# Kernel optimization log

Hardware: AMD Instinct MI355X
Metric: run time of the kernel (lower is better)

## Reference

```python
import jax, jax.numpy as jnp
import numpy as np

N, E, G, H = 4096, 8192, 64, 128  # nodes, edges, graphs, hidden dim
NODE_DIM, EDGE_DIM = 11, 5


def _linear_params(key, fan_in, fan_out):
    kw, kb = jax.random.split(key)
    s = 1.0 / np.sqrt(fan_in)
    w = jax.random.uniform(kw, (fan_in, fan_out), minval=-s, maxval=s, dtype=jnp.float32)
    b = jax.random.uniform(kb, (fan_out,), minval=-s, maxval=s, dtype=jnp.float32)
    return w, b


def setup_inputs() -> dict:
    key = jax.random.key(0)
    ks = jax.random.split(key, 10)
    x = jax.random.normal(ks[0], (N, NODE_DIM), dtype=jnp.float32)
    edge_attr = jax.random.normal(ks[1], (E, EDGE_DIM), dtype=jnp.float32)
    edge_index = jax.random.randint(ks[2], (2, E), 0, N, dtype=jnp.int64)
    batch = jnp.sort(jax.random.randint(ks[3], (N,), 0, G, dtype=jnp.int64))
    # preprocess MLP: node_dim -> 128 -> 128
    p1_w, p1_b = _linear_params(ks[4], NODE_DIM, H)
    p2_w, p2_b = _linear_params(ks[5], H, H)
    # edge net: edge_dim -> 128 -> 256 -> 128 -> 128*128 (ReLU between, none after last)
    e1_w, e1_b = _linear_params(ks[6], EDGE_DIM, 128)
    e2_w, e2_b = _linear_params(ks[7], 128, 256)
    e3_w, e3_b = _linear_params(ks[8], 256, 128)
    e4_w, e4_b = _linear_params(ks[9], 128, H * H)
    return {"x": x, "edge_attr": edge_attr, "edge_index": edge_index, "batch": batch,
            "p1_w": p1_w, "p1_b": p1_b, "p2_w": p2_w, "p2_b": p2_b,
            "e1_w": e1_w, "e1_b": e1_b, "e2_w": e2_w, "e2_b": e2_b,
            "e3_w": e3_w, "e3_b": e3_b, "e4_w": e4_w, "e4_b": e4_b}


def reference(x, edge_attr, edge_index, batch,
              p1_w, p1_b, p2_w, p2_b,
              e1_w, e1_b, e2_w, e2_b, e3_w, e3_b, e4_w, e4_b):
    # node preprocess MLP (maps 11-dim features to 128 so NNConv dims are consistent)
    h = jax.nn.relu(x @ p1_w + p1_b) @ p2_w + p2_b  # [N, H]
    # edge network -> per-edge weight matrix [E, H, H]
    e = jax.nn.relu(edge_attr @ e1_w + e1_b)
    e = jax.nn.relu(e @ e2_w + e2_b)
    e = jax.nn.relu(e @ e3_w + e3_b)
    W = (e @ e4_w + e4_b).reshape(E, H, H)
    # NNConv (root_weight=False, bias=False, aggr='mean'):
    src, dst = edge_index[0], edge_index[1]
    msg = jnp.einsum('ei,eio->eo', h[src], W)  # gather + per-edge matmul, [E, H]
    agg = jax.ops.segment_sum(msg, dst, num_segments=N)
    cnt = jax.ops.segment_sum(jnp.ones((E,), msg.dtype), dst, num_segments=N)
    h_out = agg / jnp.maximum(cnt, 1.0)[:, None]  # scatter-mean, [N, H]
    # global add pool over graphs
    pooled = jax.ops.segment_sum(h_out, batch, num_segments=G)  # [G, H]
    return pooled
```

## Files before the change

### kernel.cpp

```cpp
#include <hip/hip_runtime.h>
#include <hip/hip_bf16.h>

#define N_NODES 4096
#define N_EDGES 8192
#define N_GRAPHS 64
#define HDIM 128

typedef __attribute__((ext_vector_type(8))) short bf16x8;
typedef __attribute__((ext_vector_type(4))) float f32x4;

static __device__ __forceinline__ unsigned short f2bf(float f) {
    unsigned u = __builtin_bit_cast(unsigned, f);
    u += 0x7fffu + ((u >> 16) & 1u);
    return (unsigned short)(u >> 16);
}
static __device__ __forceinline__ float bf2f(unsigned short s) {
    unsigned u = ((unsigned)s) << 16;
    return __builtin_bit_cast(float, u);
}

__global__ __launch_bounds__(256) void pre_kernel(
    const float* __restrict__ x, const float* __restrict__ p1w, const float* __restrict__ p1b,
    const float* __restrict__ p2w, const float* __restrict__ p2b, const float* __restrict__ e4b,
    unsigned short* __restrict__ h_bf, float* __restrict__ hb,
    const float* __restrict__ w4, unsigned short* __restrict__ w4perm,
    const float* __restrict__ w2, unsigned short* __restrict__ w2p,
    const float* __restrict__ w3, unsigned short* __restrict__ w3p)
{
    __shared__ __align__(16) char smem[33024];
    const int t = threadIdx.x;
    const int bid = blockIdx.x;

    if (bid < 256) {
        float (*xs)[11]  = (float(*)[11])smem;
        float (*l1t)[16] = (float(*)[16])(smem + 704);
        float (*hs)[16]  = (float(*)[16])(smem + 8896);
        const int nb = bid;

        for (int r = t; r < 16 * 11; r += 256) {
            int e = r / 11, d = r % 11;
            xs[e][d] = x[(nb * 16 + e) * 11 + d];
        }
        __syncthreads();
        {
            int j = t & 127;
            float wd[11];
            #pragma unroll
            for (int d = 0; d < 11; ++d) wd[d] = p1w[d * 128 + j];
            float bj = p1b[j];
            for (int p = 0; p < 8; ++p) {
                int e = p * 2 + (t >> 7);
                float acc = bj;
                #pragma unroll
                for (int d = 0; d < 11; ++d) acc += xs[e][d] * wd[d];
                l1t[j][e] = fmaxf(acc, 0.f);
            }
        }
        __syncthreads();
        {
            int j = t & 127, eh = t >> 7;
            float acc[8];
            float bj = p2b[j];
            #pragma unroll
            for (int r = 0; r < 8; ++r) acc[r] = bj;
            #pragma unroll 8
            for (int k = 0; k < 128; ++k) {
                float w = p2w[k * 128 + j];
                const float4* row = (const float4*)&l1t[k][eh * 8];
                float4 v0 = row[0], v1 = row[1];
                acc[0] += v0.x * w; acc[1] += v0.y * w; acc[2] += v0.z * w; acc[3] += v0.w * w;
                acc[4] += v1.x * w; acc[5] += v1.y * w; acc[6] += v1.z * w; acc[7] += v1.w * w;
            }
            #pragma unroll
            for (int r = 0; r < 8; ++r) {
                int e = eh * 8 + r;
                h_bf[(nb * 16 + e) * 128 + j] = f2bf(acc[r]);
                hs[j][e] = acc[r];
            }
        }
        __syncthreads();
        {
            int j = t & 127, eh = t >> 7;
            float acc[8] = {0.f,0.f,0.f,0.f,0.f,0.f,0.f,0.f};
            #pragma unroll 8
            for (int i = 0; i < 128; ++i) {
                float w = e4b[i * 128 + j];
                const float4* row = (const float4*)&hs[i][eh * 8];
                float4 v0 = row[0], v1 = row[1];
                acc[0] += v0.x * w; acc[1] += v0.y * w; acc[2] += v0.z * w; acc[3] += v0.w * w;
                acc[4] += v1.x * w; acc[5] += v1.y * w; acc[6] += v1.z * w; acc[7] += v1.w * w;
            }
            #pragma unroll
            for (int r = 0; r < 8; ++r) hb[(nb * 16 + eh * 8 + r) * 128 + j] = acc[r];
        }
    } else if (bid < 384) {
        unsigned short (*tt)[129] = (unsigned short(*)[129])smem;
        const int i = bid - 256;
        for (int r = t; r < 16384; r += 256) {
            int k = r >> 7, o = r & 127;
            tt[o][k] = f2bf(w4[k * 16384 + i * 128 + o]);
        }
        __syncthreads();
        for (int r = t; r < 16384; r += 256) {
            int o = r >> 7, k = r & 127;
            w4perm[((size_t)(o >> 5) * 128 + i) * 4352 + (size_t)(o & 31) * 136 + k] = tt[o][k];
        }
    } else if (bid < 386) {
        unsigned short (*tt)[129] = (unsigned short(*)[129])smem;
        const int oh = bid - 384;
        for (int r = t; r < 16384; r += 256) {
            int k = r >> 7, ol = r & 127;
            tt[ol][k] = f2bf(w2[k * 256 + oh * 128 + ol]);
        }
        __syncthreads();
        for (int r = t; r < 16384; r += 256) {
            int ol = r >> 7, k = r & 127;
            w2p[(oh * 128 + ol) * 136 + k] = tt[ol][k];
        }
    } else {
        unsigned short (*tt)[257] = (unsigned short(*)[257])smem;
        const int oh = bid - 386;
        for (int r = t; r < 16384; r += 256) {
            int k = r >> 6, ol = r & 63;
            tt[ol][k] = f2bf(w3[k * 128 + oh * 64 + ol]);
        }
        __syncthreads();
        for (int r = t; r < 16384; r += 256) {
            int ol = r >> 8, k = r & 255;
            w3p[(oh * 64 + ol) * 264 + k] = tt[ol][k];
        }
    }
}

__global__ __launch_bounds__(256, 2) void edge23_kernel(
    const float* __restrict__ ea, const float* __restrict__ w1, const float* __restrict__ b1,
    const float* __restrict__ b2, const float* __restrict__ b3,
    const unsigned short* __restrict__ w2p, const unsigned short* __restrict__ w3p,
    unsigned short* __restrict__ e3bf, float* __restrict__ aggz)
{
    const int t = threadIdx.x, bid = blockIdx.x;

    if (bid >= 512) {
        float4* dst = (float4*)aggz;
        const float4 z = make_float4(0.f, 0.f, 0.f, 0.f);
        for (int i = (bid - 512) * 256 + t; i < 132096; i += 128 * 256) dst[i] = z;
        return;
    }

    __shared__ __align__(16) float es[16][5];
    __shared__ __align__(16) unsigned short l1a[16 * 136];
    __shared__ __align__(16) unsigned short l2a[16 * 264];
    const int w = t >> 6, lane = t & 63, q = lane >> 4, l15 = lane & 15;
    const int e0 = bid * 16;
    const f32x4 zero4 = (f32x4){0.f, 0.f, 0.f, 0.f};

    for (int r = t; r < 80; r += 256) es[r / 5][r % 5] = ea[e0 * 5 + r];
    __syncthreads();
    {
        int j = t & 127, eh = t >> 7;
        float wd[5];
        #pragma unroll
        for (int d = 0; d < 5; ++d) wd[d] = w1[d * 128 + j];
        float bj = b1[j];
        #pragma unroll
        for (int p = 0; p < 8; ++p) {
            int e = eh * 8 + p;
            float acc = bj;
            #pragma unroll
            for (int d = 0; d < 5; ++d) acc += es[e][d] * wd[d];
            l1a[e * 136 + j] = f2bf(fmaxf(acc, 0.f));
        }
    }
    __syncthreads();

    bf16x8 afrag[4];
    #pragma unroll
    for (int s = 0; s < 4; ++s)
        afrag[s] = *(const bf16x8*)&l1a[l15 * 136 + s * 32 + q * 8];

    f32x4 acc[4];
    #pragma unroll
    for (int ob = 0; ob < 4; ++ob) acc[ob] = zero4;
    #pragma unroll
    for (int ob = 0; ob < 4; ++ob) {
        const int o = w * 64 + ob * 16 + l15;
        bf16x8 bfrag[4];
        #pragma unroll
        for (int s = 0; s < 4; ++s)
            bfrag[s] = *(const bf16x8*)(w2p + (size_t)o * 136 + s * 32 + q * 8);
        f32x4 tmp = __builtin_amdgcn_mfma_f32_16x16x32_bf16(afrag[0], bfrag[0], zero4, 0, 0, 0);
        tmp = __builtin_amdgcn_mfma_f32_16x16x32_bf16(afrag[1], bfrag[1], tmp, 0, 0, 0);
        tmp = __builtin_amdgcn_mfma_f32_16x16x32_bf16(afrag[2], bfrag[2], tmp, 0, 0, 0);
        acc[ob] = __builtin_amdgcn_mfma_f32_16x16x32_bf16(afrag[3], bfrag[3], tmp, 0, 0, 0);
    }
    #pragma unroll
    for (int ob = 0; ob < 4; ++ob) {
        int o = w * 64 + ob * 16 + l15;
        float bo = b2[o];
        #pragma unroll
        for (int r = 0; r < 4; ++r) {
            int e_loc = q * 4 + r;
            l2a[e_loc * 264 + o] = f2bf(fmaxf(acc[ob][r] + bo, 0.f));
        }
    }
    __syncthreads();

    f32x4 acc3[2];
    acc3[0] = zero4; acc3[1] = zero4;
    #pragma unroll
    for (int ks = 0; ks < 8; ++ks) {
        bf16x8 a3 = *(const bf16x8*)&l2a[l15 * 264 + ks * 32 + q * 8];
        #pragma unroll
        for (int ob = 0; ob < 2; ++ob) {
            const int o = w * 32 + ob * 16 + l15;
            bf16x8 bf = *(const bf16x8*)(w3p + (size_t)o * 264 + ks * 32 + q * 8);
            acc3[ob] = __builtin_amdgcn_mfma_f32_16x16x32_bf16(a3, bf, acc3[ob], 0, 0, 0);
        }
    }
    #pragma unroll
    for (int ob = 0; ob < 2; ++ob) {
        int o = w * 32 + ob * 16 + l15;
        float bo = b3[o];
        #pragma unroll
        for (int r = 0; r < 4; ++r) {
            int e = e0 + q * 4 + r;
            e3bf[(size_t)e * 128 + o] = f2bf(fmaxf(acc3[ob][r] + bo, 0.f));
        }
    }
}

__global__ __launch_bounds__(256, 3) void nnconv_kernel(
    const unsigned short* __restrict__ e3bf, const unsigned short* __restrict__ h_bf,
    const unsigned short* __restrict__ w4perm, const float* __restrict__ hb,
    const int* __restrict__ ei, float* __restrict__ agg, float* __restrict__ cnt)
{
    __shared__ __align__(16) float ht_f[64 * 64];
    __shared__ __align__(16) float red[2 * 64 * 16];
    const int t = threadIdx.x;
    const int bid = blockIdx.x;
    const int osplit = bid & 3;
    const int ksplit = (bid >> 2) & 1;
    const int etile  = bid >> 3;
    const int w = t >> 6, lane = t & 63, q = lane >> 4, l15 = lane & 15;
    const int og   = w & 1;
    const int kpar = w >> 1;
    const int e0 = etile * 64;
    const int o0 = osplit * 32;
    const int i0 = ksplit * 64;

    bf16x8 afrag[4][4];
    #pragma unroll
    for (int mb = 0; mb < 4; ++mb)
        #pragma unroll
        for (int s = 0; s < 4; ++s) {
            int row = e0 + mb * 16 + l15;
            afrag[mb][s] = *(const bf16x8*)(e3bf + (size_t)row * 128 + s * 32 + q * 8);
        }
    #pragma unroll
    for (int mb = 0; mb < 4; ++mb)
        #pragma unroll
        for (int s = 0; s < 4; ++s)
            asm volatile("" : "+v"(afrag[mb][s]));
    asm volatile("" ::: "memory");

    {
        int r = t >> 2, part = t & 3;
        int s = ei[e0 + r];
        #pragma unroll
        for (int u = 0; u < 2; ++u) {
            uint4 v = *(const uint4*)(h_bf + (size_t)s * 128 + i0 + part * 16 + u * 8);
            const unsigned short* pv = (const unsigned short*)&v;
            #pragma unroll
            for (int j = 0; j < 8; ++j)
                ht_f[(part * 16 + u * 8 + j) * 64 + r] = bf2f(pv[j]);
        }
    }

    f32x4 acc[4];
    #pragma unroll
    for (int mb = 0; mb < 4; ++mb) acc[mb] = (f32x4){0.f, 0.f, 0.f, 0.f};
    const f32x4 zero4 = (f32x4){0.f, 0.f, 0.f, 0.f};

    __syncthreads();

    const unsigned short* bbase =
        w4perm + ((size_t)osplit * 128 + i0 + kpar * 32) * 4352
               + (size_t)(og * 16 + l15) * 136 + q * 8;
    #pragma unroll 2
    for (int c = 0; c < 32; ++c) {
        const unsigned short* bp = bbase + (size_t)c * 4352;
        bf16x8 bfrag[4];
        #pragma unroll
        for (int s = 0; s < 4; ++s)
            bfrag[s] = *(const bf16x8*)(bp + s * 32);
        const int cg = kpar * 32 + c;
        #pragma unroll
        for (int mb = 0; mb < 4; ++mb) {
            f32x4 hv = *(const f32x4*)&ht_f[cg * 64 + mb * 16 + q * 4];
            f32x4 tmp = __builtin_amdgcn_mfma_f32_16x16x32_bf16(afrag[mb][0], bfrag[0], zero4, 0, 0, 0);
            tmp = __builtin_amdgcn_mfma_f32_16x16x32_bf16(afrag[mb][1], bfrag[1], tmp, 0, 0, 0);
            tmp = __builtin_amdgcn_mfma_f32_16x16x32_bf16(afrag[mb][2], bfrag[2], tmp, 0, 0, 0);
            tmp = __builtin_amdgcn_mfma_f32_16x16x32_bf16(afrag[mb][3], bfrag[3], tmp, 0, 0, 0);
            #pragma unroll
            for (int r = 0; r < 4; ++r)
                acc[mb][r] += hv[r] * tmp[r];
        }
    }

    if (kpar == 1) {
        #pragma unroll
        for (int mb = 0; mb < 4; ++mb)
            #pragma unroll
            for (int r = 0; r < 4; ++r)
                red[(og * 64 + mb * 16 + q * 4 + r) * 16 + l15] = acc[mb][r];
    }
    __syncthreads();
    if (kpar == 0) {
        #pragma unroll
        for (int mb = 0; mb < 4; ++mb) {
            #pragma unroll
            for (int r = 0; r < 4; ++r) {
                int e_loc = mb * 16 + q * 4 + r;
                int e = e0 + e_loc;
                int de = ei[N_EDGES + e];
                int se = ei[e];
                int o = o0 + og * 16 + l15;
                float v = acc[mb][r] + red[(og * 64 + e_loc) * 16 + l15];
                if (ksplit == 0) v += hb[(size_t)se * 128 + o];
                if (osplit == 0 && ksplit == 0 && og == 0 && l15 == 0)
                    atomicAdd(&cnt[de], 1.0f);
                atomicAdd(&agg[(size_t)de * 128 + o], v);
            }
        }
    }
}

__global__ __launch_bounds__(128) void pool_kernel(
    const float* __restrict__ agg, const float* __restrict__ cnt,
    const int* __restrict__ batch, float* __restrict__ out)
{
    const int g = blockIdx.x, t = threadIdx.x;
    int lo = 0, hi = N_NODES;
    while (lo < hi) { int m = (lo + hi) >> 1; if (batch[m] < g) lo = m + 1; else hi = m; }
    const int n_lo = lo;
    int lo2 = n_lo, hi2 = N_NODES;
    while (lo2 < hi2) { int m = (lo2 + hi2) >> 1; if (batch[m] < g + 1) lo2 = m + 1; else hi2 = m; }
    const int n_hi = lo2;

    float s0 = 0.f, s1 = 0.f, s2 = 0.f, s3 = 0.f;
    int n = n_lo;
    for (; n + 4 <= n_hi; n += 4) {
        float c0 = cnt[n], c1 = cnt[n + 1], c2 = cnt[n + 2], c3 = cnt[n + 3];
        float v0 = agg[(n    ) * 128 + t];
        float v1 = agg[(n + 1) * 128 + t];
        float v2 = agg[(n + 2) * 128 + t];
        float v3 = agg[(n + 3) * 128 + t];
        s0 += v0 / (c0 > 1.f ? c0 : 1.f);
        s1 += v1 / (c1 > 1.f ? c1 : 1.f);
        s2 += v2 / (c2 > 1.f ? c2 : 1.f);
        s3 += v3 / (c3 > 1.f ? c3 : 1.f);
    }
    for (; n < n_hi; ++n) {
        float c = cnt[n];
        s0 += agg[n * 128 + t] / (c > 1.f ? c : 1.f);
    }
    out[g * 128 + t] = (s0 + s1) + (s2 + s3);
}

extern "C" void kernel_launch(void* const* d_in, const int* in_sizes, int n_in,
                              void* d_out, int out_size, void* d_ws, size_t ws_size,
                              hipStream_t stream)
{
    const float* x     = (const float*)d_in[0];
    const float* ea    = (const float*)d_in[1];
    const int*   ei    = (const int*)d_in[2];
    const int*   batch = (const int*)d_in[3];
    const float* p1w   = (const float*)d_in[4];
    const float* p1b   = (const float*)d_in[5];
    const float* p2w   = (const float*)d_in[6];
    const float* p2b   = (const float*)d_in[7];
    const float* w1    = (const float*)d_in[8];
    const float* b1    = (const float*)d_in[9];
    const float* w2    = (const float*)d_in[10];
    const float* b2    = (const float*)d_in[11];
    const float* w3    = (const float*)d_in[12];
    const float* b3    = (const float*)d_in[13];
    const float* w4    = (const float*)d_in[14];
    const float* b4    = (const float*)d_in[15];
    float* out = (float*)d_out;
    (void)in_sizes; (void)n_in; (void)out_size; (void)ws_size;

    char* ws = (char*)d_ws;
    unsigned short* h_bf = (unsigned short*)(ws);
    unsigned short* e3bf = (unsigned short*)(ws + 1048576);
    float* hb            = (float*)(ws + 3145728);
    unsigned short* w4p  = (unsigned short*)(ws + 5242880);
    float* agg           = (float*)(ws + 9699328);
    float* cnt           = (float*)(ws + 11796480);
    unsigned short* w2p  = (unsigned short*)(ws + 11812864);
    unsigned short* w3p  = (unsigned short*)(ws + 11882496);

    pre_kernel<<<388, 256, 0, stream>>>(
        x, p1w, p1b, p2w, p2b, b4, h_bf, hb,
        w4, w4p, w2, w2p, w3, w3p);
    edge23_kernel<<<640, 256, 0, stream>>>(ea, w1, b1, b2, b3, w2p, w3p, e3bf, agg);
    nnconv_kernel<<<1024, 256, 0, stream>>>(e3bf, h_bf, w4p, hb, ei, agg, cnt);
    pool_kernel<<<N_GRAPHS, 128, 0, stream>>>(agg, cnt, batch, out);
}
```

Measured before the change: 176.3 us.

## Fuse edge MLP into preprocessing kernel and widen pool kernel

Merges the edge-network layers 1-3 into the preprocessing kernel as extra blocks. This removes one kernel launch and the separate W2/W3 transpose-to-bf16 pass: the edge blocks now read fp32 W2/W3 straight from global memory with strided scalar loads and convert them on the fly. The agg zeroing also moves into the fused kernel. The pool kernel goes from 128 to 512 threads per graph, with node rows split across 4 thread groups and reduced through shared memory. The trade-off is that each of the 512 edge blocks now repeats uncoalesced strided weight loads and conversions instead of loading pre-packed bf16 vectors.

```diff
diff --git a/kernel.cpp b/kernel.cpp
--- a/kernel.cpp
+++ b/kernel.cpp
@@ -19,23 +19,115 @@
     return __builtin_bit_cast(float, u);
 }
 
-__global__ __launch_bounds__(256) void pre_kernel(
+__global__ __launch_bounds__(256) void fused_pre_edge_kernel(
     const float* __restrict__ x, const float* __restrict__ p1w, const float* __restrict__ p1b,
     const float* __restrict__ p2w, const float* __restrict__ p2b, const float* __restrict__ e4b,
     unsigned short* __restrict__ h_bf, float* __restrict__ hb,
+    const float* __restrict__ ea, const float* __restrict__ w1, const float* __restrict__ b1,
+    const float* __restrict__ w2, const float* __restrict__ b2,
+    const float* __restrict__ w3, const float* __restrict__ b3,
+    unsigned short* __restrict__ e3bf,
     const float* __restrict__ w4, unsigned short* __restrict__ w4perm,
-    const float* __restrict__ w2, unsigned short* __restrict__ w2p,
-    const float* __restrict__ w3, unsigned short* __restrict__ w3p)
+    float* __restrict__ aggz)
 {
     __shared__ __align__(16) char smem[33024];
     const int t = threadIdx.x;
     const int bid = blockIdx.x;
 
-    if (bid < 256) {
+    if (bid < 512) {
+        float (*es)[5] = (float(*)[5])smem;
+        unsigned short* l1a = (unsigned short*)(smem + 320);
+        unsigned short* l2a = (unsigned short*)(smem + 4672);
+        const int w = t >> 6, lane = t & 63, q = lane >> 4, l15 = lane & 15;
+        const int e0 = bid * 16;
+        const f32x4 zero4 = (f32x4){0.f, 0.f, 0.f, 0.f};
+
+        for (int r = t; r < 80; r += 256) es[r / 5][r % 5] = ea[e0 * 5 + r];
+        __syncthreads();
+        {
+            int j = t & 127, eh = t >> 7;
+            float wd[5];
+            #pragma unroll
+            for (int d = 0; d < 5; ++d) wd[d] = w1[d * 128 + j];
+            float bj = b1[j];
+            #pragma unroll
+            for (int p = 0; p < 8; ++p) {
+                int e = eh * 8 + p;
+                float acc = bj;
+                #pragma unroll
+                for (int d = 0; d < 5; ++d) acc += es[e][d] * wd[d];
+                l1a[e * 136 + j] = f2bf(fmaxf(acc, 0.f));
+            }
+        }
+        __syncthreads();
+
+        bf16x8 afrag[4];
+        #pragma unroll
+        for (int s = 0; s < 4; ++s)
+            afrag[s] = *(const bf16x8*)&l1a[l15 * 136 + s * 32 + q * 8];
+
+        f32x4 acc[4];
+        #pragma unroll
+        for (int ob = 0; ob < 4; ++ob) acc[ob] = zero4;
+        #pragma unroll
+        for (int ob = 0; ob < 4; ++ob) {
+            const int o = w * 64 + ob * 16 + l15;
+            bf16x8 bfrag[4];
+            #pragma unroll
+            for (int s = 0; s < 4; ++s) {
+                const int kb = s * 32 + q * 8;
+                #pragma unroll
+                for (int kk = 0; kk < 8; ++kk)
+                    bfrag[s][kk] = (short)f2bf(w2[(kb + kk) * 256 + o]);
+            }
+            f32x4 tmp = __builtin_amdgcn_mfma_f32_16x16x32_bf16(afrag[0], bfrag[0], zero4, 0, 0, 0);
+            tmp = __builtin_amdgcn_mfma_f32_16x16x32_bf16(afrag[1], bfrag[1], tmp, 0, 0, 0);
+            tmp = __builtin_amdgcn_mfma_f32_16x16x32_bf16(afrag[2], bfrag[2], tmp, 0, 0, 0);
+            acc[ob] = __builtin_amdgcn_mfma_f32_16x16x32_bf16(afrag[3], bfrag[3], tmp, 0, 0, 0);
+        }
+        #pragma unroll
+        for (int ob = 0; ob < 4; ++ob) {
+            int o = w * 64 + ob * 16 + l15;
+            float bo = b2[o];
+            #pragma unroll
+            for (int r = 0; r < 4; ++r) {
+                int e_loc = q * 4 + r;
+                l2a[e_loc * 264 + o] = f2bf(fmaxf(acc[ob][r] + bo, 0.f));
+            }
+        }
+        __syncthreads();
+
+        f32x4 acc3[2];
+        acc3[0] = zero4; acc3[1] = zero4;
+        #pragma unroll
+        for (int ks = 0; ks < 8; ++ks) {
+            bf16x8 a3 = *(const bf16x8*)&l2a[l15 * 264 + ks * 32 + q * 8];
+            #pragma unroll
+            for (int ob = 0; ob < 2; ++ob) {
+                const int o = w * 32 + ob * 16 + l15;
+                bf16x8 bf;
+                const int kb = ks * 32 + q * 8;
+                #pragma unroll
+                for (int kk = 0; kk < 8; ++kk)
+                    bf[kk] = (short)f2bf(w3[(kb + kk) * 128 + o]);
+                acc3[ob] = __builtin_amdgcn_mfma_f32_16x16x32_bf16(a3, bf, acc3[ob], 0, 0, 0);
+            }
+        }
+        #pragma unroll
+        for (int ob = 0; ob < 2; ++ob) {
+            int o = w * 32 + ob * 16 + l15;
+            float bo = b3[o];
+            #pragma unroll
+            for (int r = 0; r < 4; ++r) {
+                int e = e0 + q * 4 + r;
+                e3bf[(size_t)e * 128 + o] = f2bf(fmaxf(acc3[ob][r] + bo, 0.f));
+            }
+        }
+    } else if (bid < 768) {
         float (*xs)[11]  = (float(*)[11])smem;
         float (*l1t)[16] = (float(*)[16])(smem + 704);
         float (*hs)[16]  = (float(*)[16])(smem + 8896);
-        const int nb = bid;
+        const int nb = bid - 512;
 
         for (int r = t; r < 16 * 11; r += 256) {
             int e = r / 11, d = r % 11;
@@ -93,9 +185,9 @@
             #pragma unroll
             for (int r = 0; r < 8; ++r) hb[(nb * 16 + eh * 8 + r) * 128 + j] = acc[r];
         }
-    } else if (bid < 384) {
+    } else if (bid < 896) {
         unsigned short (*tt)[129] = (unsigned short(*)[129])smem;
-        const int i = bid - 256;
+        const int i = bid - 768;
         for (int r = t; r < 16384; r += 256) {
             int k = r >> 7, o = r & 127;
             tt[o][k] = f2bf(w4[k * 16384 + i * 128 + o]);
@@ -105,127 +197,10 @@
             int o = r >> 7, k = r & 127;
             w4perm[((size_t)(o >> 5) * 128 + i) * 4352 + (size_t)(o & 31) * 136 + k] = tt[o][k];
         }
-    } else if (bid < 386) {
-        unsigned short (*tt)[129] = (unsigned short(*)[129])smem;
-        const int oh = bid - 384;
-        for (int r = t; r < 16384; r += 256) {
-            int k = r >> 7, ol = r & 127;
-            tt[ol][k] = f2bf(w2[k * 256 + oh * 128 + ol]);
-        }
-        __syncthreads();
-        for (int r = t; r < 16384; r += 256) {
-            int ol = r >> 7, k = r & 127;
-            w2p[(oh * 128 + ol) * 136 + k] = tt[ol][k];
-        }
     } else {
-        unsigned short (*tt)[257] = (unsigned short(*)[257])smem;
-        const int oh = bid - 386;
-        for (int r = t; r < 16384; r += 256) {
-            int k = r >> 6, ol = r & 63;
-            tt[ol][k] = f2bf(w3[k * 128 + oh * 64 + ol]);
-        }
-        __syncthreads();
-        for (int r = t; r < 16384; r += 256) {
-            int ol = r >> 8, k = r & 255;
-            w3p[(oh * 64 + ol) * 264 + k] = tt[ol][k];
-        }
-    }
-}
-
-__global__ __launch_bounds__(256, 2) void edge23_kernel(
-    const float* __restrict__ ea, const float* __restrict__ w1, const float* __restrict__ b1,
-    const float* __restrict__ b2, const float* __restrict__ b3,
-    const unsigned short* __restrict__ w2p, const unsigned short* __restrict__ w3p,
-    unsigned short* __restrict__ e3bf, float* __restrict__ aggz)
-{
-    const int t = threadIdx.x, bid = blockIdx.x;
-
-    if (bid >= 512) {
         float4* dst = (float4*)aggz;
         const float4 z = make_float4(0.f, 0.f, 0.f, 0.f);
-        for (int i = (bid - 512) * 256 + t; i < 132096; i += 128 * 256) dst[i] = z;
-        return;
-    }
-
-    __shared__ __align__(16) float es[16][5];
-    __shared__ __align__(16) unsigned short l1a[16 * 136];
-    __shared__ __align__(16) unsigned short l2a[16 * 264];
-    const int w = t >> 6, lane = t & 63, q = lane >> 4, l15 = lane & 15;
-    const int e0 = bid * 16;
-    const f32x4 zero4 = (f32x4){0.f, 0.f, 0.f, 0.f};
-
-    for (int r = t; r < 80; r += 256) es[r / 5][r % 5] = ea[e0 * 5 + r];
-    __syncthreads();
-    {
-        int j = t & 127, eh = t >> 7;
-        float wd[5];
-        #pragma unroll
-        for (int d = 0; d < 5; ++d) wd[d] = w1[d * 128 + j];
-        float bj = b1[j];
-        #pragma unroll
-        for (int p = 0; p < 8; ++p) {
-            int e = eh * 8 + p;
-            float acc = bj;
-            #pragma unroll
-            for (int d = 0; d < 5; ++d) acc += es[e][d] * wd[d];
-            l1a[e * 136 + j] = f2bf(fmaxf(acc, 0.f));
-        }
-    }
-    __syncthreads();
-
-    bf16x8 afrag[4];
-    #pragma unroll
-    for (int s = 0; s < 4; ++s)
-        afrag[s] = *(const bf16x8*)&l1a[l15 * 136 + s * 32 + q * 8];
-
-    f32x4 acc[4];
-    #pragma unroll
-    for (int ob = 0; ob < 4; ++ob) acc[ob] = zero4;
-    #pragma unroll
-    for (int ob = 0; ob < 4; ++ob) {
-        const int o = w * 64 + ob * 16 + l15;
-        bf16x8 bfrag[4];
-        #pragma unroll
-        for (int s = 0; s < 4; ++s)
-            bfrag[s] = *(const bf16x8*)(w2p + (size_t)o * 136 + s * 32 + q * 8);
-        f32x4 tmp = __builtin_amdgcn_mfma_f32_16x16x32_bf16(afrag[0], bfrag[0], zero4, 0, 0, 0);
-        tmp = __builtin_amdgcn_mfma_f32_16x16x32_bf16(afrag[1], bfrag[1], tmp, 0, 0, 0);
-        tmp = __builtin_amdgcn_mfma_f32_16x16x32_bf16(afrag[2], bfrag[2], tmp, 0, 0, 0);
-        acc[ob] = __builtin_amdgcn_mfma_f32_16x16x32_bf16(afrag[3], bfrag[3], tmp, 0, 0, 0);
-    }
-    #pragma unroll
-    for (int ob = 0; ob < 4; ++ob) {
-        int o = w * 64 + ob * 16 + l15;
-        float bo = b2[o];
-        #pragma unroll
-        for (int r = 0; r < 4; ++r) {
-            int e_loc = q * 4 + r;
-            l2a[e_loc * 264 + o] = f2bf(fmaxf(acc[ob][r] + bo, 0.f));
-        }
-    }
-    __syncthreads();
-
-    f32x4 acc3[2];
-    acc3[0] = zero4; acc3[1] = zero4;
-    #pragma unroll
-    for (int ks = 0; ks < 8; ++ks) {
-        bf16x8 a3 = *(const bf16x8*)&l2a[l15 * 264 + ks * 32 + q * 8];
-        #pragma unroll
-        for (int ob = 0; ob < 2; ++ob) {
-            const int o = w * 32 + ob * 16 + l15;
-            bf16x8 bf = *(const bf16x8*)(w3p + (size_t)o * 264 + ks * 32 + q * 8);
-            acc3[ob] = __builtin_amdgcn_mfma_f32_16x16x32_bf16(a3, bf, acc3[ob], 0, 0, 0);
-        }
-    }
-    #pragma unroll
-    for (int ob = 0; ob < 2; ++ob) {
-        int o = w * 32 + ob * 16 + l15;
-        float bo = b3[o];
-        #pragma unroll
-        for (int r = 0; r < 4; ++r) {
-            int e = e0 + q * 4 + r;
-            e3bf[(size_t)e * 128 + o] = f2bf(fmaxf(acc3[ob][r] + bo, 0.f));
-        }
+        for (int i = (bid - 896) * 256 + t; i < 132096; i += 128 * 256) dst[i] = z;
     }
 }
 
@@ -335,11 +310,13 @@
     }
 }
 
-__global__ __launch_bounds__(128) void pool_kernel(
+__global__ __launch_bounds__(512) void pool_kernel(
     const float* __restrict__ agg, const float* __restrict__ cnt,
     const int* __restrict__ batch, float* __restrict__ out)
 {
-    const int g = blockIdx.x, t = threadIdx.x;
+    __shared__ float ps[4][128];
+    const int g = blockIdx.x;
+    const int ch = threadIdx.x & 127, th = threadIdx.x >> 7;
     int lo = 0, hi = N_NODES;
     while (lo < hi) { int m = (lo + hi) >> 1; if (batch[m] < g) lo = m + 1; else hi = m; }
     const int n_lo = lo;
@@ -347,24 +324,16 @@
     while (lo2 < hi2) { int m = (lo2 + hi2) >> 1; if (batch[m] < g + 1) lo2 = m + 1; else hi2 = m; }
     const int n_hi = lo2;
 
-    float s0 = 0.f, s1 = 0.f, s2 = 0.f, s3 = 0.f;
-    int n = n_lo;
-    for (; n + 4 <= n_hi; n += 4) {
-        float c0 = cnt[n], c1 = cnt[n + 1], c2 = cnt[n + 2], c3 = cnt[n + 3];
-        float v0 = agg[(n    ) * 128 + t];
-        float v1 = agg[(n + 1) * 128 + t];
-        float v2 = agg[(n + 2) * 128 + t];
-        float v3 = agg[(n + 3) * 128 + t];
-        s0 += v0 / (c0 > 1.f ? c0 : 1.f);
-        s1 += v1 / (c1 > 1.f ? c1 : 1.f);
-        s2 += v2 / (c2 > 1.f ? c2 : 1.f);
-        s3 += v3 / (c3 > 1.f ? c3 : 1.f);
-    }
-    for (; n < n_hi; ++n) {
+    float s = 0.f;
+    for (int n = n_lo + th; n < n_hi; n += 4) {
         float c = cnt[n];
-        s0 += agg[n * 128 + t] / (c > 1.f ? c : 1.f);
-    }
-    out[g * 128 + t] = (s0 + s1) + (s2 + s3);
+        c = c > 1.f ? c : 1.f;
+        s += agg[n * 128 + ch] / c;
+    }
+    ps[th][ch] = s;
+    __syncthreads();
+    if (th == 0)
+        out[g * 128 + ch] = (ps[0][ch] + ps[1][ch]) + (ps[2][ch] + ps[3][ch]);
 }
 
 extern "C" void kernel_launch(void* const* d_in, const int* in_sizes, int n_in,
@@ -397,13 +366,11 @@
     unsigned short* w4p  = (unsigned short*)(ws + 5242880);
     float* agg           = (float*)(ws + 9699328);
     float* cnt           = (float*)(ws + 11796480);
-    unsigned short* w2p  = (unsigned short*)(ws + 11812864);
-    unsigned short* w3p  = (unsigned short*)(ws + 11882496);
-
-    pre_kernel<<<388, 256, 0, stream>>>(
+
+    fused_pre_edge_kernel<<<1024, 256, 0, stream>>>(
         x, p1w, p1b, p2w, p2b, b4, h_bf, hb,
-        w4, w4p, w2, w2p, w3, w3p);
-    edge23_kernel<<<640, 256, 0, stream>>>(ea, w1, b1, b2, b3, w2p, w3p, e3bf, agg);
+        ea, w1, b1, w2, b2, w3, b3, e3bf,
+        w4, w4p, agg);
     nnconv_kernel<<<1024, 256, 0, stream>>>(e3bf, h_bf, w4p, hb, ei, agg, cnt);
-    pool_kernel<<<N_GRAPHS, 128, 0, stream>>>(agg, cnt, batch, out);
-}
+    pool_kernel<<<N_GRAPHS, 512, 0, stream>>>(agg, cnt, batch, out);
+}
```

Result: faster. 169.5 us (median of 3 runs) (-3.9%).
